# Optimization experiments

Hardware: AMD Instinct MI355X
Metric: run time of the kernel (lower is better)

The kernel has to match this reference:

```python
import jax, jax.numpy as jnp
import numpy as np

EPS = 1e-5
MIN_NORM = 1e-10

def _norm(x):
    return jnp.sqrt(jnp.clip(jnp.sum(x * x, axis=-1, keepdims=True), MIN_NORM, None))

def _proj(x):
    # clip points to the open unit Poincare ball
    n = _norm(x)
    max_n = 1.0 - EPS
    return jnp.where(n > max_n, x * (max_n / n), x)

def _artanh(x):
    return jnp.arctanh(jnp.clip(x, -1.0 + EPS, 1.0 - EPS))

def mob_add(u, v):
    uv = jnp.sum(u * v, axis=-1, keepdims=True)
    u2 = jnp.sum(u * u, axis=-1, keepdims=True)
    v2 = jnp.sum(v * v, axis=-1, keepdims=True)
    num = (1.0 + 2.0 * uv + v2) * u + (1.0 - u2) * v
    den = 1.0 + 2.0 * uv + u2 * v2
    return _proj(num / jnp.maximum(den, MIN_NORM))

def mob_mat_mul(M, x):
    # M: [Din, Dout], x: [B, Din] on the ball. Ganea Mobius matvec.
    x = _proj(x)
    Mx = x @ M
    x_n = _norm(x)
    Mx_n = _norm(Mx)
    return _proj(jnp.tanh(Mx_n / x_n * _artanh(x_n)) * (Mx / Mx_n))

def log_map_zero(y):
    n = _norm(y)
    return _artanh(n) * y / n

def exp_map_zero(v):
    n = _norm(v)
    return _proj(jnp.tanh(n) * v / n)

def mob_pointwise_prod(x, u):
    # coordinate-wise scale of hyperbolic x by gate u, in the tangent space at 0
    return exp_map_zero(log_map_zero(x) * u)

def _transition(W, h, U, x, b):
    Wh = mob_mat_mul(W, h)
    Ux = mob_mat_mul(U, x)
    return mob_add(mob_add(Wh, Ux), b)

def setup_inputs() -> dict:
    B, I, H = 2048, 1024, 1024
    Din, Dh = 2 * I, 2 * H
    k = (1.0 / H) ** 0.5
    key = jax.random.key(0)
    ks = jax.random.split(key, 8)
    return {
        "hyp_x": jax.random.normal(ks[0], (B, Din), jnp.float32) * 0.01,
        "hidden": jax.random.normal(ks[1], (B, Dh), jnp.float32) * 0.01,
        "w_z": jax.random.uniform(ks[2], (Dh, Dh), jnp.float32, -k, k),
        "w_r": jax.random.uniform(ks[3], (Dh, Dh), jnp.float32, -k, k),
        "w_h": jax.random.uniform(ks[4], (Dh, Dh), jnp.float32, -k, k),
        "u_z": jax.random.uniform(ks[5], (Din, Dh), jnp.float32, -k, k),
        "u_r": jax.random.uniform(ks[6], (Din, Dh), jnp.float32, -k, k),
        "b_z": jnp.zeros((Dh,), jnp.float32),
        "b_r": jnp.zeros((Dh,), jnp.float32),
        "b_h": jnp.zeros((Dh,), jnp.float32),
    }

def reference(hyp_x, hidden, w_z, w_r, w_h, u_z, u_r, b_z, b_r, b_h):
    hyp_x = _proj(hyp_x)
    hidden = _proj(hidden)
    z = jax.nn.sigmoid(log_map_zero(_transition(w_z, hidden, u_z, hyp_x, b_z)))
    r = jax.nn.sigmoid(log_map_zero(_transition(w_r, hidden, u_r, hyp_x, b_r)))
    r_point_h = mob_pointwise_prod(hidden, r)
    # NOTE: original source uses u_r (not u_h) here; replicated faithfully.
    h_tilde = _transition(w_h, r_point_h, u_r, hyp_x, b_h)
    minus_h_oplus_htilde = mob_add(-hidden, h_tilde)
    new_h = mob_add(hidden, mob_pointwise_prod(minus_h_oplus_htilde, z))
    return new_h
```

## Files before the change

kernel.cpp:

```cpp
#include <hip/hip_runtime.h>
#include <hip/hip_bf16.h>
#include <math.h>

#define EPS 1e-5f
#define MAXN (1.0f - EPS)
#define MINN 1e-10f

constexpr int D = 2048;

typedef unsigned short u16;
typedef __bf16 bf16x8 __attribute__((ext_vector_type(8)));
typedef float floatx4 __attribute__((ext_vector_type(4)));


__device__ __forceinline__ u16 f2bf(float f) {
    union { float f; unsigned u; } v; v.f = f;
    unsigned r = v.u + 0x7FFFu + ((v.u >> 16) & 1u);
    return (u16)(r >> 16);
}

__device__ __forceinline__ float bf2f(u16 b) {
    union { unsigned u; float f; } v; v.u = ((unsigned)b) << 16; return v.f;
}

__device__ __forceinline__ void load_bf8(const u16* p, float* d) {
    uint4 r = *(const uint4*)p;
    unsigned w[4] = {r.x, r.y, r.z, r.w};
    #pragma unroll
    for (int i = 0; i < 4; ++i) {
        d[2 * i]     = bf2f((u16)(w[i] & 0xFFFFu));
        d[2 * i + 1] = bf2f((u16)(w[i] >> 16));
    }
}

__device__ __forceinline__ void store_bf8(u16* p, const float* s) {
    u16 pk[8];
    #pragma unroll
    for (int i = 0; i < 8; ++i) pk[i] = f2bf(s[i]);
    *(uint4*)p = *(const uint4*)pk;
}

__device__ __forceinline__ void load_f8(const float* p, float* d) {
    *(float4*)(d)     = *(const float4*)(p);
    *(float4*)(d + 4) = *(const float4*)(p + 4);
}

__device__ __forceinline__ void store_f8(float* p, const float* s) {
    *(float4*)(p)     = *(const float4*)(s);
    *(float4*)(p + 4) = *(const float4*)(s + 4);
}

__device__ __forceinline__ float artanh_(float x) {
    x = fminf(fmaxf(x, -1.0f + EPS), 1.0f - EPS);
    return 0.5f * logf((1.0f + x) / (1.0f - x));
}

__device__ __forceinline__ float sigmoid_(float x) {
    return 1.0f / (1.0f + expf(-x));
}

__device__ __forceinline__ void gl_lds16(const u16* g, u16* l) {
    __builtin_amdgcn_global_load_lds(
        (const __attribute__((address_space(1))) unsigned int*)g,
        (__attribute__((address_space(3))) unsigned int*)l, 16, 0, 0);
}

template<int N>
__device__ __forceinline__ void block_sums(float* v, float* sbuf) {
    #pragma unroll
    for (int n = 0; n < N; ++n)
        #pragma unroll
        for (int off = 32; off >= 1; off >>= 1) v[n] += __shfl_xor(v[n], off, 64);
    int w = threadIdx.x >> 6;
    __syncthreads();
    if ((threadIdx.x & 63) == 0) {
        #pragma unroll
        for (int n = 0; n < N; ++n) sbuf[w * N + n] = v[n];
    }
    __syncthreads();
    #pragma unroll
    for (int n = 0; n < N; ++n)
        v[n] = sbuf[n] + sbuf[N + n] + sbuf[2 * N + n] + sbuf[3 * N + n];
}

__device__ __forceinline__ void mmm_finish(float sum2, float g, float* coef, float* onorm) {
    float mxn = sqrtf(fmaxf(sum2, MINN));
    float tt  = tanhf(mxn * g);
    float on  = fminf(tt, MAXN);
    *coef = on / mxn;
    *onorm = on;
}

__device__ __forceinline__ float mob_apply(float* u, const float* v,
                                           float u2, float v2, float duv) {
    float cu  = 1.f + 2.f * duv + v2;
    float cv  = 1.f - u2;
    float den = fmaxf(1.f + 2.f * duv + u2 * v2, MINN);
    float s2  = cu * cu * u2 + 2.f * cu * cv * duv + cv * cv * v2;
    float n   = sqrtf(fmaxf(s2 / (den * den), MINN));
    float sc  = ((n > MAXN) ? MAXN / n : 1.f) / den;
    #pragma unroll
    for (int i = 0; i < 8; ++i) u[i] = sc * (cu * u[i] + cv * v[i]);
    return fminf(n, MAXN);
}


struct PrepBatch {
    const float* W[5]; u16* Wt[5];
    const float* hx; const float* h;
    u16* hx_bf; u16* h_bf;
    float* g_x; float* g_h;
};

__global__ __launch_bounds__(256) void wtrans_prep(PrepBatch pb) {
    __shared__ float tile[64 * 65];
    int t = threadIdx.x;

    if (blockIdx.z < 5) {
        const float* W = pb.W[blockIdx.z];
        u16* Wt = pb.Wt[blockIdx.z];
        int n0 = blockIdx.x * 64, k0 = blockIdx.y * 64;

        int lr = t >> 4, lc = (t & 15) * 4;
        #pragma unroll
        for (int p = 0; p < 4; ++p) {
            int r = lr + p * 16;
            float4 v = *(const float4*)(W + (size_t)(k0 + r) * D + n0 + lc);
            tile[r * 65 + lc + 0] = v.x;
            tile[r * 65 + lc + 1] = v.y;
            tile[r * 65 + lc + 2] = v.z;
            tile[r * 65 + lc + 3] = v.w;
        }
        __syncthreads();

        int wn = t >> 3, ws = (t & 7) * 8;
        #pragma unroll
        for (int p = 0; p < 2; ++p) {
            int n = wn + p * 32;
            u16 pk[8];
            #pragma unroll
            for (int j = 0; j < 8; ++j) pk[j] = f2bf(tile[(ws + j) * 65 + n]);
            *(uint4*)(Wt + (size_t)(n0 + n) * D + k0 + ws) = *(uint4*)pk;
        }
    } else {
        int bid = blockIdx.y * (D / 64) + blockIdx.x;
        for (int rr = 0; rr < 2; ++rr) {
            int b = bid * 2 + rr;
            size_t off = (size_t)b * D + t * 8;
            float xv[8], hv[8];
            load_f8(pb.hx + off, xv);
            load_f8(pb.h + off, hv);
            float s[2] = {0.f, 0.f};
            #pragma unroll
            for (int i = 0; i < 8; ++i) { s[0] += xv[i] * xv[i]; s[1] += hv[i] * hv[i]; }
            block_sums<2>(s, tile);

            float nx = sqrtf(fmaxf(s[0], MINN));
            float scx = (nx > MAXN) ? MAXN / nx : 1.0f;
            float nh = sqrtf(fmaxf(s[1], MINN));
            float sch = (nh > MAXN) ? MAXN / nh : 1.0f;
            #pragma unroll
            for (int i = 0; i < 8; ++i) { xv[i] *= scx; hv[i] *= sch; }
            store_bf8(pb.hx_bf + off, xv);
            store_bf8(pb.h_bf + off, hv);
            if (t == 0) {
                float xn = fminf(nx, MAXN), hn = fminf(nh, MAXN);
                pb.g_x[b] = artanh_(xn) / xn;
                pb.g_h[b] = artanh_(hn) / hn;
            }
        }
    }
}


struct GemmBatch { const u16* A[4]; const u16* W[4]; void* C[4]; int koff[4]; };

template<int KLEN, typename CT>
__global__ __launch_bounds__(256) void gemm_bt(GemmBatch gb) {
    int z = blockIdx.z;
    const u16* __restrict__ A = gb.A[z];
    const u16* __restrict__ W = gb.W[z];
    CT* __restrict__ C = (CT*)gb.C[z];
    int koff = gb.koff[z];

    __shared__ u16 As[128 * 64];
    __shared__ u16 Ws[128 * 64];

    int t = threadIdx.x;
    int wave = t >> 6, lane = t & 63;
    int wr = wave >> 1, wc = wave & 1;
    int quad = lane >> 4, l16 = lane & 15;
    int brow = blockIdx.y * 128, bcol = blockIdx.x * 128;

    int srow = 32 * wave + (lane >> 3);
    int sseg = (lane & 7) ^ ((lane >> 3) & 7);
    const u16* pa = A + (size_t)(brow + srow) * D + koff + sseg * 8;
    const u16* pw = W + (size_t)(bcol + srow) * D + koff + sseg * 8;
    u16* lbA = &As[wave * 2048];
    u16* lbW = &Ws[wave * 2048];

    floatx4 acc[4][4];
    #pragma unroll
    for (int i = 0; i < 4; ++i)
        #pragma unroll
        for (int j = 0; j < 4; ++j)
            #pragma unroll
            for (int e = 0; e < 4; ++e) acc[i][j][e] = 0.f;

    int xsw = l16 & 7;

    for (int k0 = 0; k0 < KLEN; k0 += 64) {
        __syncthreads();
        #pragma unroll
        for (int i = 0; i < 4; ++i) {
            gl_lds16(pa + (size_t)(8 * i) * D + k0, lbA + i * 512);
            gl_lds16(pw + (size_t)(8 * i) * D + k0, lbW + i * 512);
        }
        __syncthreads();

        #pragma unroll
        for (int kk = 0; kk < 2; ++kk) {
            bf16x8 af[4], bfv[4];
            int ps = ((kk * 4 + quad) ^ xsw) * 8;
            #pragma unroll
            for (int i = 0; i < 4; ++i)
                af[i] = *(const bf16x8*)(&As[(wr * 64 + i * 16 + l16) * 64 + ps]);
            #pragma unroll
            for (int j = 0; j < 4; ++j)
                bfv[j] = *(const bf16x8*)(&Ws[(wc * 64 + j * 16 + l16) * 64 + ps]);
            #pragma unroll
            for (int i = 0; i < 4; ++i)
                #pragma unroll
                for (int j = 0; j < 4; ++j)
                    acc[i][j] = __builtin_amdgcn_mfma_f32_16x16x32_bf16(af[i], bfv[j], acc[i][j], 0, 0, 0);
        }
    }

    #pragma unroll
    for (int i = 0; i < 4; ++i) {
        #pragma unroll
        for (int j = 0; j < 4; ++j) {
            int row = brow + wr * 64 + i * 16 + quad * 4;
            int col = bcol + wc * 64 + j * 16 + l16;
            #pragma unroll
            for (int r = 0; r < 4; ++r) {
                float val = acc[i][j][r];
                if constexpr (sizeof(CT) == 2)
                    C[(size_t)(row + r) * D + col] = (CT)f2bf(val);
                else
                    C[(size_t)(row + r) * D + col] = (CT)val;
            }
        }
    }
}


__global__ __launch_bounds__(256) void mid_kernel(
    const u16* __restrict__ c_wz, const u16* __restrict__ c_uz,
    const u16* __restrict__ c_wr, const u16* __restrict__ c_ur,
    const u16* __restrict__ h_bf,
    const float* __restrict__ g_x, const float* __restrict__ g_h,
    const float* __restrict__ b_z, const float* __restrict__ b_r,
    u16* __restrict__ z_out, u16* __restrict__ uxr_out,
    u16* __restrict__ rph_bf, float* __restrict__ g_rph) {
    __shared__ float sbuf[24];
    int b = blockIdx.x, t = threadIdx.x;
    size_t off = (size_t)b * D + t * 8;
    int cbase = t * 8;

    float wz[8], uz[8], wr2[8], ur2[8], hp[8], bz[8], br[8];
    load_bf8(c_wz + off, wz);
    load_bf8(c_uz + off, uz);
    load_bf8(c_wr + off, wr2);
    load_bf8(c_ur + off, ur2);
    load_bf8(h_bf + off, hp);
    load_f8(b_z + cbase, bz);
    load_f8(b_r + cbase, br);

    float s[6] = {0, 0, 0, 0, 0, 0};
    #pragma unroll
    for (int i = 0; i < 8; ++i) {
        s[0] += wz[i] * wz[i];  s[1] += uz[i] * uz[i];
        s[2] += wr2[i] * wr2[i]; s[3] += ur2[i] * ur2[i];
        s[4] += bz[i] * bz[i];  s[5] += br[i] * br[i];
    }
    block_sums<6>(s, sbuf);
    float gh = g_h[b], gx = g_x[b];

    float cwz, nwz, cuz, nuz, cwr, nwr, cur, nur;
    mmm_finish(s[0], gh, &cwz, &nwz);
    mmm_finish(s[1], gx, &cuz, &nuz);
    mmm_finish(s[2], gh, &cwr, &nwr);
    mmm_finish(s[3], gx, &cur, &nur);
    #pragma unroll
    for (int i = 0; i < 8; ++i) {
        wz[i] *= cwz; uz[i] *= cuz; wr2[i] *= cwr; ur2[i] *= cur;
    }
    float sbz = s[4], sbr2 = s[5];

    float d[2] = {0.f, 0.f};
    #pragma unroll
    for (int i = 0; i < 8; ++i) { d[0] += wz[i] * uz[i]; d[1] += wr2[i] * ur2[i]; }
    block_sums<2>(d, sbuf);
    float n1z = mob_apply(wz, uz, nwz * nwz, nuz * nuz, d[0]);
    float n1r = mob_apply(wr2, ur2, nwr * nwr, nur * nur, d[1]);

    d[0] = 0.f; d[1] = 0.f;
    #pragma unroll
    for (int i = 0; i < 8; ++i) { d[0] += wz[i] * bz[i]; d[1] += wr2[i] * br[i]; }
    block_sums<2>(d, sbuf);
    float n2z = mob_apply(wz, bz, n1z * n1z, sbz, d[0]);
    float n2r = mob_apply(wr2, br, n1r * n1r, sbr2, d[1]);

    float gz = artanh_(n2z) / n2z;
    float gr = artanh_(n2r) / n2r;
    float zz[8], v[8];
    float sv = 0.f;
    #pragma unroll
    for (int i = 0; i < 8; ++i) {
        zz[i] = sigmoid_(gz * wz[i]);
        float r = sigmoid_(gr * wr2[i]);
        v[i] = gh * hp[i] * r;
        sv += v[i] * v[i];
    }
    store_bf8(z_out + off, zz);
    block_sums<1>(&sv, sbuf);
    float nv = sqrtf(fmaxf(sv, MINN));
    float th = fminf(tanhf(nv), MAXN);
    float cr = th / nv;
    #pragma unroll
    for (int i = 0; i < 8; ++i) v[i] *= cr;
    store_bf8(rph_bf + off, v);
    store_bf8(uxr_out + off, ur2);
    if (t == 0) g_rph[b] = artanh_(th) / th;
}


__global__ __launch_bounds__(256) void fin_kernel(
    const u16* __restrict__ p0, const u16* __restrict__ p1,
    const u16* __restrict__ p2, const u16* __restrict__ p3,
    const u16* __restrict__ uxr, const u16* __restrict__ z_in,
    const u16* __restrict__ h_bf,
    const float* __restrict__ g_rph, const float* __restrict__ b_h,
    float* __restrict__ out) {
    __shared__ float sbuf[16];
    int b = blockIdx.x, t = threadIdx.x;
    size_t off = (size_t)b * D + t * 8;
    int cbase = t * 8;

    float wh[8], ux[8], zz[8], hp[8], bh[8], t0[8], t1[8];
    load_bf8(p0 + off, wh);
    load_bf8(p1 + off, t0);
    load_bf8(p2 + off, t1);
    #pragma unroll
    for (int i = 0; i < 8; ++i) wh[i] += t0[i] + t1[i];
    load_bf8(p3 + off, t0);
    #pragma unroll
    for (int i = 0; i < 8; ++i) wh[i] += t0[i];
    load_bf8(uxr + off, ux);
    load_bf8(z_in + off, zz);
    load_bf8(h_bf + off, hp);
    load_f8(b_h + cbase, bh);

    float s[4] = {0, 0, 0, 0};
    #pragma unroll
    for (int i = 0; i < 8; ++i) {
        s[0] += wh[i] * wh[i]; s[1] += ux[i] * ux[i];
        s[2] += hp[i] * hp[i]; s[3] += bh[i] * bh[i];
    }
    block_sums<4>(s, sbuf);
    float swh = s[0], sux = s[1], shp = s[2], sbh = s[3];

    float cwh, nwh;
    mmm_finish(swh, g_rph[b], &cwh, &nwh);
    #pragma unroll
    for (int i = 0; i < 8; ++i) wh[i] *= cwh;

    float d = 0.f;
    #pragma unroll
    for (int i = 0; i < 8; ++i) d += wh[i] * ux[i];
    block_sums<1>(&d, sbuf);
    float n1 = mob_apply(wh, ux, nwh * nwh, sux, d);

    d = 0.f;
    #pragma unroll
    for (int i = 0; i < 8; ++i) d += wh[i] * bh[i];
    block_sums<1>(&d, sbuf);
    float nht = mob_apply(wh, bh, n1 * n1, sbh, d);

    #pragma unroll
    for (int i = 0; i < 8; ++i) ux[i] = -hp[i];
    d = 0.f;
    #pragma unroll
    for (int i = 0; i < 8; ++i) d += ux[i] * wh[i];
    block_sums<1>(&d, sbuf);
    float nm = mob_apply(ux, wh, shp, nht * nht, d);

    float lm = artanh_(nm) / nm;
    float sv = 0.f;
    #pragma unroll
    for (int i = 0; i < 8; ++i) {
        float v = lm * ux[i] * zz[i];
        ux[i] = v;
        sv += v * v;
    }
    block_sums<1>(&sv, sbuf);
    float nv = sqrtf(fmaxf(sv, MINN));
    float th = fminf(tanhf(nv), MAXN);
    float ce = th / nv;
    #pragma unroll
    for (int i = 0; i < 8; ++i) ux[i] *= ce;

    d = 0.f;
    #pragma unroll
    for (int i = 0; i < 8; ++i) d += hp[i] * ux[i];
    block_sums<1>(&d, sbuf);
    mob_apply(hp, ux, shp, th * th, d);
    store_f8(out + off, hp);
}


extern "C" void kernel_launch(void* const* d_in, const int* in_sizes, int n_in,
                              void* d_out, int out_size, void* d_ws, size_t ws_size,
                              hipStream_t stream) {
    const float* hyp_x  = (const float*)d_in[0];
    const float* hidden = (const float*)d_in[1];
    const float* w_z = (const float*)d_in[2];
    const float* w_r = (const float*)d_in[3];
    const float* w_h = (const float*)d_in[4];
    const float* u_z = (const float*)d_in[5];
    const float* u_r = (const float*)d_in[6];
    const float* b_z = (const float*)d_in[7];
    const float* b_r = (const float*)d_in[8];
    const float* b_h = (const float*)d_in[9];
    float* out = (float*)d_out;

    int B = in_sizes[1] / D;

    char* ws = (char*)d_ws;
    size_t o = 0;
    auto alloc = [&](size_t bytes) -> void* {
        void* p = ws + o;
        o += (bytes + 255) & ~(size_t)255;
        return p;
    };
    u16* wt[5];
    for (int i = 0; i < 5; ++i) wt[i] = (u16*)alloc((size_t)D * D * 2);
    u16* hx_bf = (u16*)alloc((size_t)B * D * 2);
    u16* h_bf  = (u16*)alloc((size_t)B * D * 2);
    float* g_x   = (float*)alloc((size_t)B * 4);
    float* g_h   = (float*)alloc((size_t)B * 4);
    float* g_rph = (float*)alloc((size_t)B * 4);
    u16* cz0 = (u16*)alloc((size_t)B * D * 2);
    u16* cz1 = (u16*)alloc((size_t)B * D * 2);
    u16* cz2 = (u16*)alloc((size_t)B * D * 2);
    u16* cz3 = (u16*)alloc((size_t)B * D * 2);
    u16* p0 = (u16*)alloc((size_t)B * D * 2);
    u16* p1 = (u16*)alloc((size_t)B * D * 2);
    u16* p2 = (u16*)alloc((size_t)B * D * 2);
    u16* p3 = (u16*)alloc((size_t)B * D * 2);
    u16* z_buf = (u16*)alloc((size_t)B * D * 2);
    u16* uxr = (u16*)alloc((size_t)B * D * 2);
    u16* rph = (u16*)alloc((size_t)B * D * 2);

    PrepBatch pb;
    pb.W[0] = w_z; pb.W[1] = w_r; pb.W[2] = w_h; pb.W[3] = u_z; pb.W[4] = u_r;
    for (int i = 0; i < 5; ++i) pb.Wt[i] = wt[i];
    pb.hx = hyp_x; pb.h = hidden;
    pb.hx_bf = hx_bf; pb.h_bf = h_bf;
    pb.g_x = g_x; pb.g_h = g_h;
    wtrans_prep<<<dim3(D / 64, D / 64, 6), 256, 0, stream>>>(pb);

    GemmBatch g1;
    g1.A[0] = h_bf;  g1.W[0] = wt[0]; g1.C[0] = cz0;
    g1.A[1] = hx_bf; g1.W[1] = wt[3]; g1.C[1] = cz1;
    g1.A[2] = h_bf;  g1.W[2] = wt[1]; g1.C[2] = cz2;
    g1.A[3] = hx_bf; g1.W[3] = wt[4]; g1.C[3] = cz3;
    for (int i = 0; i < 4; ++i) g1.koff[i] = 0;
    gemm_bt<2048, u16><<<dim3(D / 128, B / 128, 4), 256, 0, stream>>>(g1);

    mid_kernel<<<dim3(B), 256, 0, stream>>>(cz0, cz1, cz2, cz3, h_bf, g_x, g_h,
                                            b_z, b_r, z_buf, uxr, rph, g_rph);

    GemmBatch g2;
    u16* pbuf[4] = {p0, p1, p2, p3};
    for (int s = 0; s < 4; ++s) {
        g2.A[s] = rph; g2.W[s] = wt[2]; g2.C[s] = pbuf[s]; g2.koff[s] = s * 512;
    }
    gemm_bt<512, u16><<<dim3(D / 128, B / 128, 4), 256, 0, stream>>>(g2);

    fin_kernel<<<dim3(B), 256, 0, stream>>>(p0, p1, p2, p3, uxr, z_buf, h_bf,
                                            g_rph, b_h, out);
}
```

Before: 315.5 us.

## Overlap w_h transpose with first GEMM and halve second GEMM split-K

The w_h transpose/bf16 conversion moves out of the prep kernel and into extra blocks (z=4) of the first GEMM launch, so it runs alongside the gate GEMMs instead of on the prep critical path. The second GEMM's split-K drops from 4 slices of 512 to 2 slices of 1024. This removes two partial-sum buffers and their reads in the final kernel. In exchange, the second GEMM launches fewer blocks (512 vs 1024), which may reduce occupancy. The transpose blocks in the first GEMM also do less work than GEMM blocks, which can leave the tail unbalanced.

```diff
diff --git a/kernel.cpp b/kernel.cpp
--- a/kernel.cpp
+++ b/kernel.cpp
@@ -104,9 +104,34 @@
     return fminf(n, MAXN);
 }
 
+__device__ __forceinline__ void trans_tile(const float* W, u16* Wt,
+                                           int n0, int k0, float* tile) {
+    int t = threadIdx.x;
+    int lr = t >> 4, lc = (t & 15) * 4;
+    #pragma unroll
+    for (int p = 0; p < 4; ++p) {
+        int r = lr + p * 16;
+        float4 v = *(const float4*)(W + (size_t)(k0 + r) * D + n0 + lc);
+        tile[r * 65 + lc + 0] = v.x;
+        tile[r * 65 + lc + 1] = v.y;
+        tile[r * 65 + lc + 2] = v.z;
+        tile[r * 65 + lc + 3] = v.w;
+    }
+    __syncthreads();
+    int wn = t >> 3, ws = (t & 7) * 8;
+    #pragma unroll
+    for (int p = 0; p < 2; ++p) {
+        int n = wn + p * 32;
+        u16 pk[8];
+        #pragma unroll
+        for (int j = 0; j < 8; ++j) pk[j] = f2bf(tile[(ws + j) * 65 + n]);
+        *(uint4*)(Wt + (size_t)(n0 + n) * D + k0 + ws) = *(uint4*)pk;
+    }
+}
+
 
 struct PrepBatch {
-    const float* W[5]; u16* Wt[5];
+    const float* W[4]; u16* Wt[4];
     const float* hx; const float* h;
     u16* hx_bf; u16* h_bf;
     float* g_x; float* g_h;
@@ -116,32 +141,9 @@
     __shared__ float tile[64 * 65];
     int t = threadIdx.x;
 
-    if (blockIdx.z < 5) {
-        const float* W = pb.W[blockIdx.z];
-        u16* Wt = pb.Wt[blockIdx.z];
-        int n0 = blockIdx.x * 64, k0 = blockIdx.y * 64;
-
-        int lr = t >> 4, lc = (t & 15) * 4;
-        #pragma unroll
-        for (int p = 0; p < 4; ++p) {
-            int r = lr + p * 16;
-            float4 v = *(const float4*)(W + (size_t)(k0 + r) * D + n0 + lc);
-            tile[r * 65 + lc + 0] = v.x;
-            tile[r * 65 + lc + 1] = v.y;
-            tile[r * 65 + lc + 2] = v.z;
-            tile[r * 65 + lc + 3] = v.w;
-        }
-        __syncthreads();
-
-        int wn = t >> 3, ws = (t & 7) * 8;
-        #pragma unroll
-        for (int p = 0; p < 2; ++p) {
-            int n = wn + p * 32;
-            u16 pk[8];
-            #pragma unroll
-            for (int j = 0; j < 8; ++j) pk[j] = f2bf(tile[(ws + j) * 65 + n]);
-            *(uint4*)(Wt + (size_t)(n0 + n) * D + k0 + ws) = *(uint4*)pk;
-        }
+    if (blockIdx.z < 4) {
+        trans_tile(pb.W[blockIdx.z], pb.Wt[blockIdx.z],
+                   blockIdx.x * 64, blockIdx.y * 64, tile);
     } else {
         int bid = blockIdx.y * (D / 64) + blockIdx.x;
         for (int rr = 0; rr < 2; ++rr) {
@@ -173,19 +175,11 @@
 }
 
 
-struct GemmBatch { const u16* A[4]; const u16* W[4]; void* C[4]; int koff[4]; };
-
 template<int KLEN, typename CT>
-__global__ __launch_bounds__(256) void gemm_bt(GemmBatch gb) {
-    int z = blockIdx.z;
-    const u16* __restrict__ A = gb.A[z];
-    const u16* __restrict__ W = gb.W[z];
-    CT* __restrict__ C = (CT*)gb.C[z];
-    int koff = gb.koff[z];
-
-    __shared__ u16 As[128 * 64];
-    __shared__ u16 Ws[128 * 64];
-
+__device__ __forceinline__ void gemm_body(const u16* __restrict__ A,
+                                          const u16* __restrict__ W,
+                                          CT* __restrict__ C, int koff,
+                                          u16* As, u16* Ws) {
     int t = threadIdx.x;
     int wave = t >> 6, lane = t & 63;
     int wr = wave >> 1, wc = wave & 1;
@@ -252,6 +246,39 @@
             }
         }
     }
+}
+
+
+struct G1Batch {
+    const u16* A[4]; const u16* W[4]; u16* C[4];
+    const float* Wh; u16* WhT;
+};
+
+__global__ __launch_bounds__(256) void g1_kernel(G1Batch gb) {
+    __shared__ u16 smem[128 * 64 * 2];
+    if (blockIdx.z < 4) {
+        gemm_body<2048, u16>(gb.A[blockIdx.z], gb.W[blockIdx.z], gb.C[blockIdx.z],
+                             0, smem, smem + 128 * 64);
+    } else {
+        float* tile = (float*)smem;
+        #pragma unroll
+        for (int ti = 0; ti < 4; ++ti) {
+            if (ti) __syncthreads();
+            int n0 = (blockIdx.x * 2 + (ti & 1)) * 64;
+            int k0 = (blockIdx.y * 2 + (ti >> 1)) * 64;
+            trans_tile(gb.Wh, gb.WhT, n0, k0, tile);
+        }
+    }
+}
+
+
+struct GemmBatch { const u16* A[2]; const u16* W[2]; u16* C[2]; int koff[2]; };
+
+__global__ __launch_bounds__(256) void g2_kernel(GemmBatch gb) {
+    __shared__ u16 smem[128 * 64 * 2];
+    int z = blockIdx.z;
+    gemm_body<1024, u16>(gb.A[z], gb.W[z], gb.C[z], gb.koff[z],
+                         smem, smem + 128 * 64);
 }
 
 
@@ -338,7 +365,6 @@
 
 __global__ __launch_bounds__(256) void fin_kernel(
     const u16* __restrict__ p0, const u16* __restrict__ p1,
-    const u16* __restrict__ p2, const u16* __restrict__ p3,
     const u16* __restrict__ uxr, const u16* __restrict__ z_in,
     const u16* __restrict__ h_bf,
     const float* __restrict__ g_rph, const float* __restrict__ b_h,
@@ -348,13 +374,9 @@
     size_t off = (size_t)b * D + t * 8;
     int cbase = t * 8;
 
-    float wh[8], ux[8], zz[8], hp[8], bh[8], t0[8], t1[8];
+    float wh[8], ux[8], zz[8], hp[8], bh[8], t0[8];
     load_bf8(p0 + off, wh);
     load_bf8(p1 + off, t0);
-    load_bf8(p2 + off, t1);
-    #pragma unroll
-    for (int i = 0; i < 8; ++i) wh[i] += t0[i] + t1[i];
-    load_bf8(p3 + off, t0);
     #pragma unroll
     for (int i = 0; i < 8; ++i) wh[i] += t0[i];
     load_bf8(uxr + off, ux);
@@ -457,38 +479,36 @@
     u16* cz3 = (u16*)alloc((size_t)B * D * 2);
     u16* p0 = (u16*)alloc((size_t)B * D * 2);
     u16* p1 = (u16*)alloc((size_t)B * D * 2);
-    u16* p2 = (u16*)alloc((size_t)B * D * 2);
-    u16* p3 = (u16*)alloc((size_t)B * D * 2);
     u16* z_buf = (u16*)alloc((size_t)B * D * 2);
     u16* uxr = (u16*)alloc((size_t)B * D * 2);
     u16* rph = (u16*)alloc((size_t)B * D * 2);
 
     PrepBatch pb;
-    pb.W[0] = w_z; pb.W[1] = w_r; pb.W[2] = w_h; pb.W[3] = u_z; pb.W[4] = u_r;
-    for (int i = 0; i < 5; ++i) pb.Wt[i] = wt[i];
+    pb.W[0] = w_z; pb.Wt[0] = wt[0];
+    pb.W[1] = w_r; pb.Wt[1] = wt[1];
+    pb.W[2] = u_z; pb.Wt[2] = wt[3];
+    pb.W[3] = u_r; pb.Wt[3] = wt[4];
     pb.hx = hyp_x; pb.h = hidden;
     pb.hx_bf = hx_bf; pb.h_bf = h_bf;
     pb.g_x = g_x; pb.g_h = g_h;
-    wtrans_prep<<<dim3(D / 64, D / 64, 6), 256, 0, stream>>>(pb);
-
-    GemmBatch g1;
+    wtrans_prep<<<dim3(D / 64, D / 64, 5), 256, 0, stream>>>(pb);
+
+    G1Batch g1;
     g1.A[0] = h_bf;  g1.W[0] = wt[0]; g1.C[0] = cz0;
     g1.A[1] = hx_bf; g1.W[1] = wt[3]; g1.C[1] = cz1;
     g1.A[2] = h_bf;  g1.W[2] = wt[1]; g1.C[2] = cz2;
     g1.A[3] = hx_bf; g1.W[3] = wt[4]; g1.C[3] = cz3;
-    for (int i = 0; i < 4; ++i) g1.koff[i] = 0;
-    gemm_bt<2048, u16><<<dim3(D / 128, B / 128, 4), 256, 0, stream>>>(g1);
+    g1.Wh = w_h; g1.WhT = wt[2];
+    g1_kernel<<<dim3(D / 128, B / 128, 5), 256, 0, stream>>>(g1);
 
     mid_kernel<<<dim3(B), 256, 0, stream>>>(cz0, cz1, cz2, cz3, h_bf, g_x, g_h,
                                             b_z, b_r, z_buf, uxr, rph, g_rph);
 
     GemmBatch g2;
-    u16* pbuf[4] = {p0, p1, p2, p3};
-    for (int s = 0; s < 4; ++s) {
-        g2.A[s] = rph; g2.W[s] = wt[2]; g2.C[s] = pbuf[s]; g2.koff[s] = s * 512;
-    }
-    gemm_bt<512, u16><<<dim3(D / 128, B / 128, 4), 256, 0, stream>>>(g2);
-
-    fin_kernel<<<dim3(B), 256, 0, stream>>>(p0, p1, p2, p3, uxr, z_buf, h_bf,
+    g2.A[0] = rph; g2.W[0] = wt[2]; g2.C[0] = p0; g2.koff[0] = 0;
+    g2.A[1] = rph; g2.W[1] = wt[2]; g2.C[1] = p1; g2.koff[1] = 1024;
+    g2_kernel<<<dim3(D / 128, B / 128, 2), 256, 0, stream>>>(g2);
+
+    fin_kernel<<<dim3(B), 256, 0, stream>>>(p0, p1, uxr, z_buf, h_bf,
                                             g_rph, b_h, out);
 }
```

Measured after the change: 312.2 us. About the same (-1.0%).
